# Performance work log

Hardware: AMD Instinct MI355X
Metric: run time of the kernel (lower is better)

## Reference

```python
import jax, jax.numpy as jnp
import numpy as np

B, S, D, H = 4, 2048, 1024, 16
DH = D // H


def setup_inputs() -> dict:
    key = jax.random.key(0)
    ks = jax.random.split(key, 12)
    s = 0.02
    inp = {
        "q": jax.random.normal(ks[0], (B, S, D), jnp.float32),
        "k": jax.random.normal(ks[1], (B, S, D), jnp.float32),
        "v": jax.random.normal(ks[2], (B, S, D), jnp.float32),
        # causal mask, broadcastable over batch and heads (mask==0 -> -1e9)
        "mask": jnp.tril(jnp.ones((S, S), jnp.int32))[None, None, :, :],
        "wq": jax.random.normal(ks[3], (D, D), jnp.float32) * s,
        "bq": jnp.zeros((D,), jnp.float32),
        "wk": jax.random.normal(ks[4], (D, D), jnp.float32) * s,
        "bk": jnp.zeros((D,), jnp.float32),
        "wv": jax.random.normal(ks[5], (D, D), jnp.float32) * s,
        "bv": jnp.zeros((D,), jnp.float32),
        "wo": jax.random.normal(ks[6], (D, D), jnp.float32) * s,
        "bo": jnp.zeros((D,), jnp.float32),
    }
    return inp


def reference(q, k, v, mask, wq, bq, wk, bk, wv, bv, wo, bo):
    # linear projections (torch Linear: x @ W^T + b)
    qh = (q @ wq.T + bq).reshape(B, S, H, DH).transpose(0, 2, 1, 3)  # [B,H,S,DH]
    kh = (k @ wk.T + bk).reshape(B, S, H, DH).transpose(0, 2, 1, 3)
    vh = (v @ wv.T + bv).reshape(B, S, H, DH).transpose(0, 2, 1, 3)
    scale = 1.0 / jnp.sqrt(jnp.float32(DH))
    score = jnp.einsum("bhqd,bhkd->bhqk", qh, kh) * scale  # [B,H,S,S]
    score = jnp.where(mask == 0, jnp.float32(-1e9), score)
    attn = jax.nn.softmax(score, axis=-1)
    ctx = jnp.einsum("bhqk,bhkd->bhqd", attn, vh)  # [B,H,S,DH]
    ctx = ctx.transpose(0, 2, 1, 3).reshape(B, S, D)
    return ctx @ wo.T + bo
```

## Files before the change

kernel.cpp:

```cpp
#include <hip/hip_runtime.h>
#include <hip/hip_bf16.h>

#define NB 4
#define NS 2048
#define ND 1024
#define NH 16
#define NDH 64
#define E_ 8388608
#define W_ 1048576

typedef __attribute__((ext_vector_type(8))) __bf16 bf16x8;
typedef __attribute__((ext_vector_type(4))) float f32x4;
typedef __attribute__((ext_vector_type(16))) float f32x16;
typedef unsigned short us16;
typedef unsigned int u32;

__device__ __forceinline__ unsigned short f2bf(float f) {
  union { float f; unsigned u; } v; v.f = f;
  unsigned r = v.u + 0x7FFFu + ((v.u >> 16) & 1u);
  return (unsigned short)(r >> 16);
}

typedef const __attribute__((address_space(1))) unsigned int* gas_t;
typedef __attribute__((address_space(3))) unsigned int* las_t;
__device__ __forceinline__ void gl2lds16(const void* g, void* l) {
  __builtin_amdgcn_global_load_lds((gas_t)g, (las_t)l, 16, 0, 0);
}

__global__ __launch_bounds__(256) void conv_bf16(
    const float* __restrict__ q, const float* __restrict__ k, const float* __restrict__ v,
    const float* __restrict__ wq, const float* __restrict__ wk, const float* __restrict__ wv,
    const float* __restrict__ wo,
    us16* __restrict__ qb, us16* __restrict__ kb, us16* __restrict__ vb,
    us16* __restrict__ wqb, us16* __restrict__ wkb, us16* __restrict__ wvb,
    us16* __restrict__ wob)
{
  int b = blockIdx.x;
  int seg, off;
  if (b < 24576) { seg = b >> 13; off = b & 8191; }
  else { b -= 24576; seg = 3 + (b >> 10); off = b & 1023; }
  const float* s; us16* d;
  switch (seg) {
    case 0: s = q;  d = qb;  break;
    case 1: s = k;  d = kb;  break;
    case 2: s = v;  d = vb;  break;
    case 3: s = wq; d = wqb; break;
    case 4: s = wk; d = wkb; break;
    case 5: s = wv; d = wvb; break;
    default: s = wo; d = wob; break;
  }
  size_t idx = ((size_t)off * 256 + threadIdx.x) * 4;
  float4 f = *(const float4*)(s + idx);
  ushort4 u;
  u.x = f2bf(f.x); u.y = f2bf(f.y); u.z = f2bf(f.z); u.w = f2bf(f.w);
  *(ushort4*)(d + idx) = u;
}

__global__ __launch_bounds__(256, 3) void gemm_proj3(
    const us16* __restrict__ A0, const us16* __restrict__ A1, const us16* __restrict__ A2,
    const us16* __restrict__ W0, const us16* __restrict__ W1, const us16* __restrict__ W2,
    const float* __restrict__ b0, const float* __restrict__ b1, const float* __restrict__ b2,
    us16* __restrict__ o0, us16* __restrict__ o1, us16* __restrict__ o2,
    float qscale, int s0, int s1, int s2)
{
  const int seg = (blockIdx.z == 0) ? s0 : (blockIdx.z == 1) ? s1 : s2;
  const us16* A  = (blockIdx.z == 0) ? A0 : (blockIdx.z == 1) ? A1 : A2;
  const us16* Wt = (blockIdx.z == 0) ? W0 : (blockIdx.z == 1) ? W1 : W2;
  const float* bias = (blockIdx.z == 0) ? b0 : (blockIdx.z == 1) ? b1 : b2;
  us16* out = (blockIdx.z == 0) ? o0 : (blockIdx.z == 1) ? o1 : o2;
  const float scale = (seg == 0) ? qscale : 1.0f;

  __shared__ us16 As[128][64];
  __shared__ us16 Bs[128][64];
  const int tid = threadIdx.x;
  const int lane = tid & 63;
  const int w = tid >> 6;
  const int l15 = lane & 15, quad = lane >> 4;
  const int sw = l15 & 7;
  const int rowBase = blockIdx.x * 128, colBase = blockIdx.y * 128;
  const int srow = w * 32 + (lane >> 3);
  const int cu = (lane & 7) ^ ((lane >> 3) & 7);
  const us16* ga = A  + (size_t)(rowBase + srow) * ND + cu * 8;
  const us16* gb = Wt + (size_t)(colBase + srow) * ND + cu * 8;
  const int wr = (w >> 1) * 64, wc = (w & 1) * 64;

  f32x4 acc[4][4] = {};
  for (int kt = 0; kt < ND; kt += 64) {
    __syncthreads();
    #pragma unroll
    for (int c = 0; c < 4; ++c) {
      gl2lds16(ga + kt + c * 8 * ND, &As[w * 32 + c * 8][0]);
      gl2lds16(gb + kt + c * 8 * ND, &Bs[w * 32 + c * 8][0]);
    }
    __syncthreads();
    #pragma unroll
    for (int ks = 0; ks < 2; ++ks) {
      bf16x8 af[4], bfr[4];
      #pragma unroll
      for (int i = 0; i < 4; ++i)
        af[i]  = *(const bf16x8*)&As[wr + i * 16 + l15][((ks * 4 + quad) ^ sw) * 8];
      #pragma unroll
      for (int j = 0; j < 4; ++j)
        bfr[j] = *(const bf16x8*)&Bs[wc + j * 16 + l15][((ks * 4 + quad) ^ sw) * 8];
      #pragma unroll
      for (int i = 0; i < 4; ++i)
        #pragma unroll
        for (int j = 0; j < 4; ++j)
          acc[i][j] = __builtin_amdgcn_mfma_f32_16x16x32_bf16(af[i], bfr[j], acc[i][j], 0, 0, 0);
    }
  }

  if (seg < 2) {
    #pragma unroll
    for (int i = 0; i < 4; ++i) {
      #pragma unroll
      for (int j = 0; j < 4; ++j) {
        int colg = colBase + wc + j * 16 + l15;
        float bval = bias[colg];
        #pragma unroll
        for (int r = 0; r < 4; ++r) {
          int rowg = rowBase + wr + i * 16 + quad * 4 + r;
          out[(size_t)rowg * ND + colg] = f2bf((acc[i][j][r] + bval) * scale);
        }
      }
    }
  } else {
    #pragma unroll
    for (int i = 0; i < 4; ++i) {
      #pragma unroll
      for (int j = 0; j < 4; ++j) {
        int colg = colBase + wc + j * 16 + l15;
        float bval = bias[colg];
        int h_ = colg >> 6, d_ = colg & 63;
        int rowg0 = rowBase + wr + i * 16 + quad * 4;
        int b_ = rowg0 >> 11, sr0 = rowg0 & (NS - 1);
        ushort4 vv;
        vv.x = f2bf(acc[i][j][0] + bval);
        vv.y = f2bf(acc[i][j][1] + bval);
        vv.z = f2bf(acc[i][j][2] + bval);
        vv.w = f2bf(acc[i][j][3] + bval);
        *(ushort4*)(out + ((size_t)(b_ * NH + h_) * NDH + d_) * NS + sr0) = vv;
      }
    }
  }
}

__global__ __launch_bounds__(512, 1) void attn(
    const us16* __restrict__ Qh, const us16* __restrict__ Kh,
    const us16* __restrict__ Vht, us16* __restrict__ ctx)
{
  __shared__ us16 Ks[2][128][64];
  __shared__ us16 Vts[2][64][128];
  __shared__ float invL[8][32];

  const int bh = blockIdx.x & 63;
  const int pr = blockIdx.x >> 6;
  const int b_ = bh >> 4, h_ = bh & 15;
  const int tid = threadIdx.x, lane = tid & 63, w = tid >> 6;
  const int l31 = lane & 31;
  const int hi = lane >> 5;
  const int lr8 = lane >> 3;
  const int cu = (lane & 7) ^ (lr8 & 7);
  const int vr = lane >> 4;
  const int vs = lane & 15;
  const int cs0 = (vs & 8) | ((vs & 7) ^ vr);
  const int cs1 = (vs & 8) | ((vs & 7) ^ (vr | 4));

  const us16* gk  = Kh  + ((size_t)b_ * NS + w * 16 + lr8) * ND + h_ * NDH + cu * 8;
  const us16* gv0 = Vht + ((size_t)bh * NDH + w * 8 + vr) * NS + cs0 * 8;
  const us16* gv1 = Vht + ((size_t)bh * NDH + w * 8 + 4 + vr) * NS + cs1 * 8;

  for (int pass = 0; pass < 2; ++pass) {
    const int tq = pass ? (7 - pr) : pr;
    const int qb0 = tq * 256;
    const int nt = (tq + 1) * 2;
    const int qw = qb0 + w * 32;
    const int qg = qw + l31;

    bf16x8 bq[4];
    {
      const us16* gq = Qh + ((size_t)b_ * NS + qg) * ND + h_ * NDH + hi * 8;
      #pragma unroll
      for (int ds = 0; ds < 4; ++ds)
        bq[ds] = *(const bf16x8*)(gq + ds * 16);
    }

    __syncthreads();
    gl2lds16(gk,            &Ks[0][w * 16][0]);
    gl2lds16(gk + 8 * ND,   &Ks[0][w * 16 + 8][0]);
    gl2lds16(gv0,           &Vts[0][w * 8][0]);
    gl2lds16(gv1,           &Vts[0][w * 8 + 4][0]);

    f32x16 o0 = {}, o1 = {};
    float o_l = 0.f;

    for (int it = 0; it < nt; ++it) {
      const int kb = it * 128;
      const int cur = it & 1;
      __syncthreads();
      if (it + 1 < nt) {
        const int nxt = cur ^ 1;
        const int kn = kb + 128;
        gl2lds16(gk + (size_t)kn * ND,        &Ks[nxt][w * 16][0]);
        gl2lds16(gk + (size_t)(kn + 8) * ND,  &Ks[nxt][w * 16 + 8][0]);
        gl2lds16(gv0 + kn,                    &Vts[nxt][w * 8][0]);
        gl2lds16(gv1 + kn,                    &Vts[nxt][w * 8 + 4][0]);
      }
      #pragma unroll
      for (int kb4 = 0; kb4 < 4; ++kb4) {
        const int keyb0 = kb + kb4 * 32;
        if (keyb0 > qw + 31) continue;
        const bool full = (keyb0 + 31 <= qw);

        f32x16 c = {};
        __builtin_amdgcn_s_setprio(1);
        #pragma unroll
        for (int ds = 0; ds < 4; ++ds) {
          bf16x8 ak = *(const bf16x8*)
              &Ks[cur][kb4 * 32 + l31][(((ds * 2 + hi) ^ (l31 & 7)) * 8)];
          c = __builtin_amdgcn_mfma_f32_32x32x16_bf16(ak, bq[ds], c, 0, 0, 0);
        }
        __builtin_amdgcn_s_setprio(0);

        float p[16];
        if (full) {
          #pragma unroll
          for (int r = 0; r < 16; ++r)
            p[r] = __builtin_amdgcn_exp2f(c[r]);
        } else {
          #pragma unroll
          for (int r = 0; r < 16; ++r) {
            int kg = keyb0 + (r & 3) + 8 * (r >> 2) + 4 * hi;
            p[r] = (kg <= qg) ? __builtin_amdgcn_exp2f(c[r]) : 0.f;
          }
        }
        {
          float s0 = (p[0] + p[1]) + (p[2] + p[3]);
          float s1 = (p[4] + p[5]) + (p[6] + p[7]);
          float s2 = (p[8] + p[9]) + (p[10] + p[11]);
          float s3 = (p[12] + p[13]) + (p[14] + p[15]);
          o_l += (s0 + s1) + (s2 + s3);
        }
        u32 m[8];
        #pragma unroll
        for (int j = 0; j < 8; ++j)
          asm("v_cvt_pk_bf16_f32 %0, %1, %2" : "=v"(m[j]) : "v"(p[2 * j]), "v"(p[2 * j + 1]));
        asm volatile("v_permlane32_swap_b32 %0, %1" : "+v"(m[0]), "+v"(m[2]));
        asm volatile("v_permlane32_swap_b32 %0, %1" : "+v"(m[1]), "+v"(m[3]));
        asm volatile("v_permlane32_swap_b32 %0, %1" : "+v"(m[4]), "+v"(m[6]));
        asm volatile("v_permlane32_swap_b32 %0, %1" : "+v"(m[5]), "+v"(m[7]));
        union { u32 u[4]; bf16x8 v; } pa0, pa1;
        pa0.u[0] = m[0]; pa0.u[1] = m[1]; pa0.u[2] = m[2]; pa0.u[3] = m[3];
        pa1.u[0] = m[4]; pa1.u[1] = m[5]; pa1.u[2] = m[6]; pa1.u[3] = m[7];

        const int sw7 = l31 & 7;
        const int g0 = kb4 * 4 + hi;
        const int g1 = kb4 * 4 + 2 + hi;
        const int s00 = (g0 & 8) | ((g0 & 7) ^ sw7);
        const int s01 = (g1 & 8) | ((g1 & 7) ^ sw7);
        bf16x8 bv00 = *(const bf16x8*)&Vts[cur][l31][s00 * 8];
        bf16x8 bv01 = *(const bf16x8*)&Vts[cur][l31][s01 * 8];
        bf16x8 bv10 = *(const bf16x8*)&Vts[cur][32 + l31][s00 * 8];
        bf16x8 bv11 = *(const bf16x8*)&Vts[cur][32 + l31][s01 * 8];
        __builtin_amdgcn_s_setprio(1);
        o0 = __builtin_amdgcn_mfma_f32_32x32x16_bf16(pa0.v, bv00, o0, 0, 0, 0);
        o0 = __builtin_amdgcn_mfma_f32_32x32x16_bf16(pa1.v, bv01, o0, 0, 0, 0);
        o1 = __builtin_amdgcn_mfma_f32_32x32x16_bf16(pa0.v, bv10, o1, 0, 0, 0);
        o1 = __builtin_amdgcn_mfma_f32_32x32x16_bf16(pa1.v, bv11, o1, 0, 0, 0);
        __builtin_amdgcn_s_setprio(0);
      }
    }

    {
      float a = o_l, b = o_l;
      asm volatile("v_permlane32_swap_b32 %0, %1" : "+v"(a), "+v"(b));
      float tot = a + b;
      float inv = __builtin_amdgcn_rcpf(tot);
      if (lane < 32) invL[w][l31] = inv;
      #pragma unroll
      for (int r = 0; r < 16; ++r) {
        int qrow = (r & 3) + 8 * (r >> 2) + 4 * hi;
        float iv = invL[w][qrow];
        us16* dst = ctx + ((size_t)b_ * NS + qb0 + w * 32 + qrow) * ND + h_ * NDH + l31;
        dst[0]  = f2bf(o0[r] * iv);
        dst[32] = f2bf(o1[r] * iv);
      }
    }
  }
}

__global__ __launch_bounds__(256, 3) void gemm_out(
    const us16* __restrict__ A, const us16* __restrict__ Wt,
    const float* __restrict__ bias, float* __restrict__ out)
{
  __shared__ us16 As[128][64];
  __shared__ us16 Bs[128][64];
  const int tid = threadIdx.x;
  const int lane = tid & 63;
  const int w = tid >> 6;
  const int l15 = lane & 15, quad = lane >> 4;
  const int sw = l15 & 7;
  const int rowBase = blockIdx.x * 128, colBase = blockIdx.y * 128;
  const int srow = w * 32 + (lane >> 3);
  const int cu = (lane & 7) ^ ((lane >> 3) & 7);
  const us16* ga = A  + (size_t)(rowBase + srow) * ND + cu * 8;
  const us16* gb = Wt + (size_t)(colBase + srow) * ND + cu * 8;
  const int wr = (w >> 1) * 64, wc = (w & 1) * 64;

  f32x4 acc[4][4] = {};
  for (int kt = 0; kt < ND; kt += 64) {
    __syncthreads();
    #pragma unroll
    for (int c = 0; c < 4; ++c) {
      gl2lds16(ga + kt + c * 8 * ND, &As[w * 32 + c * 8][0]);
      gl2lds16(gb + kt + c * 8 * ND, &Bs[w * 32 + c * 8][0]);
    }
    __syncthreads();
    #pragma unroll
    for (int ks = 0; ks < 2; ++ks) {
      bf16x8 af[4], bfr[4];
      #pragma unroll
      for (int i = 0; i < 4; ++i)
        af[i]  = *(const bf16x8*)&As[wr + i * 16 + l15][((ks * 4 + quad) ^ sw) * 8];
      #pragma unroll
      for (int j = 0; j < 4; ++j)
        bfr[j] = *(const bf16x8*)&Bs[wc + j * 16 + l15][((ks * 4 + quad) ^ sw) * 8];
      #pragma unroll
      for (int i = 0; i < 4; ++i)
        #pragma unroll
        for (int j = 0; j < 4; ++j)
          acc[i][j] = __builtin_amdgcn_mfma_f32_16x16x32_bf16(af[i], bfr[j], acc[i][j], 0, 0, 0);
    }
  }

  #pragma unroll
  for (int i = 0; i < 4; ++i) {
    #pragma unroll
    for (int j = 0; j < 4; ++j) {
      int colg = colBase + wc + j * 16 + l15;
      float bval = bias[colg];
      #pragma unroll
      for (int r = 0; r < 4; ++r) {
        int rowg = rowBase + wr + i * 16 + quad * 4 + r;
        out[(size_t)rowg * ND + colg] = acc[i][j][r] + bval;
      }
    }
  }
}

extern "C" void kernel_launch(void* const* d_in, const int* in_sizes, int n_in,
                              void* d_out, int out_size, void* d_ws, size_t ws_size,
                              hipStream_t stream) {
  const float* q  = (const float*)d_in[0];
  const float* k  = (const float*)d_in[1];
  const float* v  = (const float*)d_in[2];
  const float* wq = (const float*)d_in[4];
  const float* bq_ = (const float*)d_in[5];
  const float* wk = (const float*)d_in[6];
  const float* bk_ = (const float*)d_in[7];
  const float* wv = (const float*)d_in[8];
  const float* bv_ = (const float*)d_in[9];
  const float* wo = (const float*)d_in[10];
  const float* bo_ = (const float*)d_in[11];

  us16* ws = (us16*)d_ws;
  us16* qb  = ws;
  us16* kb  = ws + (size_t)E_;
  us16* vb  = ws + (size_t)2 * E_;
  us16* wqb = ws + (size_t)3 * E_;
  us16* wkb = wqb + W_;
  us16* wvb = wkb + W_;
  us16* wob = wvb + W_;
  us16* KhF = wob + W_;
  us16* ctx = vb;
  us16* Vht = (us16*)d_out;
  us16* Qh  = (us16*)d_out + (size_t)E_;

  const float qscale = 0.125f * 1.44269504088896340736f;
  const bool fused = ws_size >= ((size_t)4 * E_ + 4 * W_) * 2;

  conv_bf16<<<28672, 256, 0, stream>>>(q, k, v, wq, wk, wv, wo,
                                       qb, kb, vb, wqb, wkb, wvb, wob);
  if (fused) {
    gemm_proj3<<<dim3(64, 8, 3), 256, 0, stream>>>(
        qb, kb, vb, wqb, wkb, wvb, bq_, bk_, bv_, Qh, KhF, Vht, qscale, 0, 1, 2);
    attn<<<256, 512, 0, stream>>>(Qh, KhF, Vht, ctx);
  } else {
    gemm_proj3<<<dim3(64, 8, 2), 256, 0, stream>>>(
        qb, vb, vb, wqb, wvb, wvb, bq_, bv_, bv_, Qh, Vht, Vht, qscale, 0, 2, 2);
    gemm_proj3<<<dim3(64, 8, 1), 256, 0, stream>>>(
        kb, kb, kb, wkb, wkb, wkb, bk_, bk_, bk_, qb, qb, qb, qscale, 1, 1, 1);
    attn<<<256, 512, 0, stream>>>(Qh, qb, Vht, ctx);
  }
  gemm_out<<<dim3(64, 8), 256, 0, stream>>>(ctx, wob, bo_, (float*)d_out);
}
```

Before: 299.8 us.

## Fuse fp32-to-bf16 conversion into projection GEMM tile loads

Removes the separate conversion kernel that wrote bf16 copies of inputs and weights. The projection and output GEMMs now load fp32 straight from global memory, pack pairs to bf16 in registers with v_cvt_pk_bf16_f32, and store the packed values into the swizzled LDS tiles. This saves a kernel launch and a full write-then-read of the bf16 buffers, but each GEMM now reads twice as many bytes per tile, gives up async global-to-LDS loads, and re-converts the same data in every block that reuses a tile. It also drops the low-workspace fallback path.

```diff
diff --git a/kernel.cpp b/kernel.cpp
--- a/kernel.cpp
+++ b/kernel.cpp
@@ -12,6 +12,7 @@
 typedef __attribute__((ext_vector_type(8))) __bf16 bf16x8;
 typedef __attribute__((ext_vector_type(4))) float f32x4;
 typedef __attribute__((ext_vector_type(16))) float f32x16;
+typedef __attribute__((ext_vector_type(4))) unsigned int u32x4;
 typedef unsigned short us16;
 typedef unsigned int u32;
 
@@ -21,51 +22,28 @@
   return (unsigned short)(r >> 16);
 }
 
+__device__ __forceinline__ u32 pk2(float lo, float hi) {
+  u32 d;
+  asm("v_cvt_pk_bf16_f32 %0, %1, %2" : "=v"(d) : "v"(lo), "v"(hi));
+  return d;
+}
+
 typedef const __attribute__((address_space(1))) unsigned int* gas_t;
 typedef __attribute__((address_space(3))) unsigned int* las_t;
 __device__ __forceinline__ void gl2lds16(const void* g, void* l) {
   __builtin_amdgcn_global_load_lds((gas_t)g, (las_t)l, 16, 0, 0);
 }
 
-__global__ __launch_bounds__(256) void conv_bf16(
-    const float* __restrict__ q, const float* __restrict__ k, const float* __restrict__ v,
-    const float* __restrict__ wq, const float* __restrict__ wk, const float* __restrict__ wv,
-    const float* __restrict__ wo,
-    us16* __restrict__ qb, us16* __restrict__ kb, us16* __restrict__ vb,
-    us16* __restrict__ wqb, us16* __restrict__ wkb, us16* __restrict__ wvb,
-    us16* __restrict__ wob)
-{
-  int b = blockIdx.x;
-  int seg, off;
-  if (b < 24576) { seg = b >> 13; off = b & 8191; }
-  else { b -= 24576; seg = 3 + (b >> 10); off = b & 1023; }
-  const float* s; us16* d;
-  switch (seg) {
-    case 0: s = q;  d = qb;  break;
-    case 1: s = k;  d = kb;  break;
-    case 2: s = v;  d = vb;  break;
-    case 3: s = wq; d = wqb; break;
-    case 4: s = wk; d = wkb; break;
-    case 5: s = wv; d = wvb; break;
-    default: s = wo; d = wob; break;
-  }
-  size_t idx = ((size_t)off * 256 + threadIdx.x) * 4;
-  float4 f = *(const float4*)(s + idx);
-  ushort4 u;
-  u.x = f2bf(f.x); u.y = f2bf(f.y); u.z = f2bf(f.z); u.w = f2bf(f.w);
-  *(ushort4*)(d + idx) = u;
-}
-
-__global__ __launch_bounds__(256, 3) void gemm_proj3(
-    const us16* __restrict__ A0, const us16* __restrict__ A1, const us16* __restrict__ A2,
-    const us16* __restrict__ W0, const us16* __restrict__ W1, const us16* __restrict__ W2,
+__global__ __launch_bounds__(256, 3) void gemm_projF(
+    const float* __restrict__ A0, const float* __restrict__ A1, const float* __restrict__ A2,
+    const float* __restrict__ W0, const float* __restrict__ W1, const float* __restrict__ W2,
     const float* __restrict__ b0, const float* __restrict__ b1, const float* __restrict__ b2,
     us16* __restrict__ o0, us16* __restrict__ o1, us16* __restrict__ o2,
     float qscale, int s0, int s1, int s2)
 {
   const int seg = (blockIdx.z == 0) ? s0 : (blockIdx.z == 1) ? s1 : s2;
-  const us16* A  = (blockIdx.z == 0) ? A0 : (blockIdx.z == 1) ? A1 : A2;
-  const us16* Wt = (blockIdx.z == 0) ? W0 : (blockIdx.z == 1) ? W1 : W2;
+  const float* A  = (blockIdx.z == 0) ? A0 : (blockIdx.z == 1) ? A1 : A2;
+  const float* Wt = (blockIdx.z == 0) ? W0 : (blockIdx.z == 1) ? W1 : W2;
   const float* bias = (blockIdx.z == 0) ? b0 : (blockIdx.z == 1) ? b1 : b2;
   us16* out = (blockIdx.z == 0) ? o0 : (blockIdx.z == 1) ? o1 : o2;
   const float scale = (seg == 0) ? qscale : 1.0f;
@@ -78,10 +56,11 @@
   const int l15 = lane & 15, quad = lane >> 4;
   const int sw = l15 & 7;
   const int rowBase = blockIdx.x * 128, colBase = blockIdx.y * 128;
-  const int srow = w * 32 + (lane >> 3);
-  const int cu = (lane & 7) ^ ((lane >> 3) & 7);
-  const us16* ga = A  + (size_t)(rowBase + srow) * ND + cu * 8;
-  const us16* gb = Wt + (size_t)(colBase + srow) * ND + cu * 8;
+  const int r8 = lane >> 3;
+  const int p8 = lane & 7;
+  const int g8 = p8 ^ r8;
+  const float* gaF = A  + (size_t)(rowBase + w * 32 + r8) * ND + g8 * 8;
+  const float* gbF = Wt + (size_t)(colBase + w * 32 + r8) * ND + g8 * 8;
   const int wr = (w >> 1) * 64, wc = (w & 1) * 64;
 
   f32x4 acc[4][4] = {};
@@ -89,8 +68,16 @@
     __syncthreads();
     #pragma unroll
     for (int c = 0; c < 4; ++c) {
-      gl2lds16(ga + kt + c * 8 * ND, &As[w * 32 + c * 8][0]);
-      gl2lds16(gb + kt + c * 8 * ND, &Bs[w * 32 + c * 8][0]);
+      const float* sa = gaF + kt + (size_t)c * 8 * ND;
+      const float* sb = gbF + kt + (size_t)c * 8 * ND;
+      f32x4 a0 = *(const f32x4*)sa, a1 = *(const f32x4*)(sa + 4);
+      f32x4 bb0 = *(const f32x4*)sb, bb1 = *(const f32x4*)(sb + 4);
+      u32x4 ua = (u32x4){pk2(a0[0], a0[1]), pk2(a0[2], a0[3]),
+                         pk2(a1[0], a1[1]), pk2(a1[2], a1[3])};
+      u32x4 ub = (u32x4){pk2(bb0[0], bb0[1]), pk2(bb0[2], bb0[3]),
+                         pk2(bb1[0], bb1[1]), pk2(bb1[2], bb1[3])};
+      *(u32x4*)&As[w * 32 + c * 8 + r8][p8 * 8] = ua;
+      *(u32x4*)&Bs[w * 32 + c * 8 + r8][p8 * 8] = ub;
     }
     __syncthreads();
     #pragma unroll
@@ -289,8 +276,8 @@
   }
 }
 
-__global__ __launch_bounds__(256, 3) void gemm_out(
-    const us16* __restrict__ A, const us16* __restrict__ Wt,
+__global__ __launch_bounds__(256, 3) void gemm_outF(
+    const us16* __restrict__ A, const float* __restrict__ Wt,
     const float* __restrict__ bias, float* __restrict__ out)
 {
   __shared__ us16 As[128][64];
@@ -303,8 +290,11 @@
   const int rowBase = blockIdx.x * 128, colBase = blockIdx.y * 128;
   const int srow = w * 32 + (lane >> 3);
   const int cu = (lane & 7) ^ ((lane >> 3) & 7);
-  const us16* ga = A  + (size_t)(rowBase + srow) * ND + cu * 8;
-  const us16* gb = Wt + (size_t)(colBase + srow) * ND + cu * 8;
+  const int r8 = lane >> 3;
+  const int p8 = lane & 7;
+  const int g8 = p8 ^ r8;
+  const us16*  ga  = A  + (size_t)(rowBase + srow) * ND + cu * 8;
+  const float* gbF = Wt + (size_t)(colBase + w * 32 + r8) * ND + g8 * 8;
   const int wr = (w >> 1) * 64, wc = (w & 1) * 64;
 
   f32x4 acc[4][4] = {};
@@ -313,7 +303,11 @@
     #pragma unroll
     for (int c = 0; c < 4; ++c) {
       gl2lds16(ga + kt + c * 8 * ND, &As[w * 32 + c * 8][0]);
-      gl2lds16(gb + kt + c * 8 * ND, &Bs[w * 32 + c * 8][0]);
+      const float* sb = gbF + kt + (size_t)c * 8 * ND;
+      f32x4 bb0 = *(const f32x4*)sb, bb1 = *(const f32x4*)(sb + 4);
+      u32x4 ub = (u32x4){pk2(bb0[0], bb0[1]), pk2(bb0[2], bb0[3]),
+                         pk2(bb1[0], bb1[1]), pk2(bb1[2], bb1[3])};
+      *(u32x4*)&Bs[w * 32 + c * 8 + r8][p8 * 8] = ub;
     }
     __syncthreads();
     #pragma unroll
@@ -364,33 +358,15 @@
   const float* bo_ = (const float*)d_in[11];
 
   us16* ws = (us16*)d_ws;
-  us16* qb  = ws;
-  us16* kb  = ws + (size_t)E_;
-  us16* vb  = ws + (size_t)2 * E_;
-  us16* wqb = ws + (size_t)3 * E_;
-  us16* wkb = wqb + W_;
-  us16* wvb = wkb + W_;
-  us16* wob = wvb + W_;
-  us16* KhF = wob + W_;
-  us16* ctx = vb;
+  us16* KhF = ws;
+  us16* ctx = ws + (size_t)E_;
   us16* Vht = (us16*)d_out;
   us16* Qh  = (us16*)d_out + (size_t)E_;
 
   const float qscale = 0.125f * 1.44269504088896340736f;
-  const bool fused = ws_size >= ((size_t)4 * E_ + 4 * W_) * 2;
-
-  conv_bf16<<<28672, 256, 0, stream>>>(q, k, v, wq, wk, wv, wo,
-                                       qb, kb, vb, wqb, wkb, wvb, wob);
-  if (fused) {
-    gemm_proj3<<<dim3(64, 8, 3), 256, 0, stream>>>(
-        qb, kb, vb, wqb, wkb, wvb, bq_, bk_, bv_, Qh, KhF, Vht, qscale, 0, 1, 2);
-    attn<<<256, 512, 0, stream>>>(Qh, KhF, Vht, ctx);
-  } else {
-    gemm_proj3<<<dim3(64, 8, 2), 256, 0, stream>>>(
-        qb, vb, vb, wqb, wvb, wvb, bq_, bv_, bv_, Qh, Vht, Vht, qscale, 0, 2, 2);
-    gemm_proj3<<<dim3(64, 8, 1), 256, 0, stream>>>(
-        kb, kb, kb, wkb, wkb, wkb, bk_, bk_, bk_, qb, qb, qb, qscale, 1, 1, 1);
-    attn<<<256, 512, 0, stream>>>(Qh, qb, Vht, ctx);
-  }
-  gemm_out<<<dim3(64, 8), 256, 0, stream>>>(ctx, wob, bo_, (float*)d_out);
-}
+
+  gemm_projF<<<dim3(64, 8, 3), 256, 0, stream>>>(
+      q, k, v, wq, wk, wv, bq_, bk_, bv_, Qh, KhF, Vht, qscale, 0, 1, 2);
+  attn<<<256, 512, 0, stream>>>(Qh, KhF, Vht, ctx);
+  gemm_outF<<<dim3(64, 8), 256, 0, stream>>>(ctx, wo, bo_, (float*)d_out);
+}
```

Measured after the change: 398.9 us. 33.1% more time.
